# Kernel optimization log

Hardware: AMD Instinct MI355X
Metric: run time of the kernel (lower is better)

Reference implementation:

```python
import jax, jax.numpy as jnp
import numpy as np

NEG_SLOPE = 0.01  # torch nn.LeakyReLU default


def _lrelu(x):
    return jax.nn.leaky_relu(x, NEG_SLOPE)


def _conv1x1(x, w):
    # x: [B,C,H,W], w: [O,C] -> [B,O,H,W]  (1x1 conv, no bias)
    return jnp.einsum('bchw,oc->bohw', x, w)


def _distance_matrix(scale, H, W, dtype):
    # even-scale branch of the torch code
    x = jnp.arange(-(scale // 2), scale // 2 + 1, dtype=dtype)  # len scale+1
    x = jnp.concatenate([x[: (scale + 1) // 2], x[(scale + 1) // 2 + 1:]])  # drop middle -> len scale
    d0 = jnp.broadcast_to(x[None, :], (scale, scale))
    d1 = d0.T
    d2 = jnp.sqrt(d0 ** 2 + d1 ** 2)
    dm = jnp.stack([d0, d1, d2], axis=0)            # [3, s, s]
    dm = jnp.tile(dm, (1, H // scale, W // scale))   # [3, H, W]
    return dm[None]                                  # [1, 3, H, W]


def setup_inputs() -> dict:
    key = jax.random.key(0)
    ks = jax.random.split(key, 10)
    B, C, h, w, scale = 1, 16, 256, 256, 4
    H, W = h * scale, w * scale
    f32 = jnp.float32

    def kaiming(k, shape):
        fan_out = shape[0]
        std = np.sqrt(2.0 / fan_out)
        return (jax.random.normal(k, shape, dtype=f32) * std)

    return {
        'lr_feature': jax.random.normal(ks[0], (B, C, h, w), dtype=f32),
        'hr_feature': jax.random.normal(ks[1], (B, C, H, W), dtype=f32),
        'w0': kaiming(ks[2], (32, 64)),
        'w1': kaiming(ks[3], (16, 32)),
        'w2': kaiming(ks[4], (8, 16)),
        'w3': kaiming(ks[5], (1, 8)),
        's0': kaiming(ks[6], (3, 3)),
        's1': kaiming(ks[7], (2, 3)),
        's2': kaiming(ks[8], (1, 2)),
        'wf': jnp.abs(kaiming(ks[9], (1, 2))),
    }


def reference(lr_feature, hr_feature, w0, w1, w2, w3, s0, s1, s2, wf):
    B, C, h, w = lr_feature.shape
    H, W = hr_feature.shape[-2:]
    scale = W // w  # static under jit

    # nearest-neighbor expand of lr_feature to hr resolution
    lr_up = jnp.repeat(jnp.repeat(lr_feature, scale, axis=2), scale, axis=3)

    # representation: [B, 4C, H, W]
    rep = jnp.concatenate(
        [lr_up, hr_feature, lr_up * hr_feature, (lr_up - hr_feature) ** 2], axis=1)

    # similarity_measure1: 4C->32->16->8->1, leaky relu after each
    o = _lrelu(_conv1x1(rep, w0))
    o = _lrelu(_conv1x1(o, w1))
    o = _lrelu(_conv1x1(o, w2))
    weights1 = _lrelu(_conv1x1(o, w3))  # [B,1,H,W]

    # similarity_measure2 on the tiled distance matrix: 3->3->2->1
    dm = _distance_matrix(scale, H, W, lr_feature.dtype)  # [1,3,H,W]
    o2 = _lrelu(_conv1x1(dm, s0))
    o2 = _lrelu(_conv1x1(o2, s1))
    weights2 = _lrelu(_conv1x1(o2, s2))  # [1,1,H,W]

    # fuse with abs-constrained weights
    fused_in = jnp.concatenate([weights1, weights2], axis=1)  # [B,2,H,W] (B=1)
    mapping = _lrelu(_conv1x1(fused_in, jnp.abs(wf)))
    return mapping
```

## Files before the change

### kernel.cpp

```cpp
#include <hip/hip_runtime.h>
#include <hip/hip_bf16.h>


typedef __attribute__((ext_vector_type(8))) short bf16x8;
typedef __attribute__((ext_vector_type(4))) short s16x4;
typedef __attribute__((ext_vector_type(4))) float f32x4;

union B8 { bf16x8 v; short2 p[4]; };
union B4 { s16x4 v; short2 p[2]; };

__device__ __forceinline__ float lrelu(float x) { return fmaxf(x, 0.01f * x); }

__device__ __forceinline__ short2 cvt2(float a, float b) {
    __hip_bfloat162 h = __float22bfloat162_rn(make_float2(a, b));
    short2 s; __builtin_memcpy(&s, &h, 4); return s;
}

__global__ __launch_bounds__(256) void ctx_mfma(
    const float* __restrict__ lr,  const float* __restrict__ hr,
    const float* __restrict__ w0g, const float* __restrict__ w1g,
    const float* __restrict__ w2g, const float* __restrict__ w3g,
    const float* __restrict__ s0g, const float* __restrict__ s1g,
    const float* __restrict__ s2g, const float* __restrict__ wfg,
    float* __restrict__ out)
{
    constexpr int W = 1024, HW = 1024 * 1024, LHW = 256 * 256;
    __shared__ __align__(16) short zbuf[4][512];

    const int tid  = threadIdx.x;
    const int lane = tid & 63;
    const int widx = tid >> 6;
    const int g    = lane >> 4;
    const int px   = lane & 15;

    const int wave_id = blockIdx.x * 4 + widx;
    const int y  = wave_id >> 3;
    const int xw = (wave_id & 7) << 7;

    B8 a1[2][2];
    #pragma unroll
    for (int m = 0; m < 2; ++m)
        #pragma unroll
        for (int q = 0; q < 2; ++q) {
            const float* wp = w0g + (m * 16 + px) * 64 + q * 32 + g * 8;
            #pragma unroll
            for (int j = 0; j < 4; ++j) a1[m][q].p[j] = cvt2(wp[2 * j], wp[2 * j + 1]);
        }
    B8 a2;
    {
        const float* wp = w1g + px * 32 + g * 8;
        #pragma unroll
        for (int j = 0; j < 4; ++j) a2.p[j] = cvt2(wp[2 * j], wp[2 * j + 1]);
    }
    B8 a3;
    {
        const bool val = (px < 8) && (g < 2);
        const float* wp = w2g + (px & 7) * 16 + (g & 1) * 8;
        const short2 z2s = make_short2(0, 0);
        #pragma unroll
        for (int j = 0; j < 4; ++j) a3.p[j] = val ? cvt2(wp[2 * j], wp[2 * j + 1]) : z2s;
    }
    const float4 w3v = *(const float4*)(w3g + (g & 1) * 4);

    const int xi = px & 3, yi = y & 3;
    const float d0 = (float)xi + ((xi < 2) ? -2.f : -1.f);
    const float d1 = (float)yi + ((yi < 2) ? -2.f : -1.f);
    const float d2 = sqrtf(d0 * d0 + d1 * d1);
    const float q0 = lrelu(s0g[0] * d0 + s0g[1] * d1 + s0g[2] * d2);
    const float q1 = lrelu(s0g[3] * d0 + s0g[4] * d1 + s0g[5] * d2);
    const float q2 = lrelu(s0g[6] * d0 + s0g[7] * d1 + s0g[8] * d2);
    const float u0 = lrelu(s1g[0] * q0 + s1g[1] * q1 + s1g[2] * q2);
    const float u1 = lrelu(s1g[3] * q0 + s1g[4] * q1 + s1g[5] * q2);
    const float wt2 = lrelu(s2g[0] * u0 + s2g[1] * u1);
    const float awf0 = fabsf(wfg[0]), awf1 = fabsf(wfg[1]);

    const int s4  = (px ^ (px >> 2)) & 3;
    short* zb = &zbuf[widx][0];
    const int row = px * 32;
    const int wza = row + ((((g >> 1)       ^ s4) & 3) << 3) + ((g & 1) << 2);
    const int wzb = row + (((((g >> 1) + 2) ^ s4) & 3) << 3) + ((g & 1) << 2);
    const int rb2 = row + (((g       ^ s4) & 3) << 3);
    const int rb3 = row + ((((g & 1) ^ s4) & 3) << 3);

    const int cb = (g & 1) << 3;
    int hr_idx[8], lr_idx[8];
    #pragma unroll
    for (int j = 0; j < 8; ++j) {
        hr_idx[j] = (cb + j) * HW  + y * W + xw + px;
        lr_idx[j] = (cb + j) * LHW + (y >> 2) * 256 + (xw >> 2) + (px >> 2);
    }
    const int oidx = y * W + xw + px;
    const bool lo = (g < 2);
    const f32x4 zf = {0.f, 0.f, 0.f, 0.f};

    #pragma unroll
    for (int tt = 0; tt < 8; ++tt) {
        float lrv[8], hrv[8];
        #pragma unroll
        for (int j = 0; j < 8; ++j) {
            hrv[j] = hr[hr_idx[j] + tt * 16];
            lrv[j] = lr[lr_idx[j] + tt * 4];
        }
        B8 b0, b1;
        #pragma unroll
        for (int j = 0; j < 4; ++j) {
            float ua = lo ? lrv[2 * j]     : hrv[2 * j];
            float ub = lo ? lrv[2 * j + 1] : hrv[2 * j + 1];
            b0.p[j] = cvt2(ua, ub);
            float da = lrv[2 * j]     - hrv[2 * j];
            float db = lrv[2 * j + 1] - hrv[2 * j + 1];
            float pa = lo ? lrv[2 * j]     * hrv[2 * j]     : da * da;
            float pb = lo ? lrv[2 * j + 1] * hrv[2 * j + 1] : db * db;
            b1.p[j] = cvt2(pa, pb);
        }
        f32x4 acc1a = __builtin_amdgcn_mfma_f32_16x16x32_bf16(a1[0][0].v, b0.v, zf, 0, 0, 0);
        acc1a = __builtin_amdgcn_mfma_f32_16x16x32_bf16(a1[0][1].v, b1.v, acc1a, 0, 0, 0);
        f32x4 acc1b = __builtin_amdgcn_mfma_f32_16x16x32_bf16(a1[1][0].v, b0.v, zf, 0, 0, 0);
        acc1b = __builtin_amdgcn_mfma_f32_16x16x32_bf16(a1[1][1].v, b1.v, acc1b, 0, 0, 0);
        B4 za, zbp;
        za.p[0]  = cvt2(lrelu(acc1a.x), lrelu(acc1a.y));
        za.p[1]  = cvt2(lrelu(acc1a.z), lrelu(acc1a.w));
        zbp.p[0] = cvt2(lrelu(acc1b.x), lrelu(acc1b.y));
        zbp.p[1] = cvt2(lrelu(acc1b.z), lrelu(acc1b.w));
        *(s16x4*)&zb[wza] = za.v;
        *(s16x4*)&zb[wzb] = zbp.v;
        bf16x8 bz1 = *(const bf16x8*)&zb[rb2];
        f32x4 acc2 = __builtin_amdgcn_mfma_f32_16x16x32_bf16(a2.v, bz1, zf, 0, 0, 0);
        B4 z2p;
        z2p.p[0] = cvt2(lrelu(acc2.x), lrelu(acc2.y));
        z2p.p[1] = cvt2(lrelu(acc2.z), lrelu(acc2.w));
        *(s16x4*)&zb[wza] = z2p.v;
        bf16x8 bz2 = *(const bf16x8*)&zb[rb3];
        f32x4 acc3 = __builtin_amdgcn_mfma_f32_16x16x32_bf16(a3.v, bz2, zf, 0, 0, 0);
        float part = w3v.x * lrelu(acc3.x) + w3v.y * lrelu(acc3.y)
                   + w3v.z * lrelu(acc3.z) + w3v.w * lrelu(acc3.w);
        float sum = part + __shfl_xor(part, 16, 64);
        float wt1 = lrelu(sum);
        float res = lrelu(awf0 * wt1 + awf1 * wt2);
        if (g == 0) out[oidx + tt * 16] = res;
    }
}

extern "C" void kernel_launch(void* const* d_in, const int* in_sizes, int n_in,
                              void* d_out, int out_size, void* d_ws, size_t ws_size,
                              hipStream_t stream) {
    const float* lr = (const float*)d_in[0];
    const float* hr = (const float*)d_in[1];
    const float* w0 = (const float*)d_in[2];
    const float* w1 = (const float*)d_in[3];
    const float* w2 = (const float*)d_in[4];
    const float* w3 = (const float*)d_in[5];
    const float* s0 = (const float*)d_in[6];
    const float* s1 = (const float*)d_in[7];
    const float* s2 = (const float*)d_in[8];
    const float* wf = (const float*)d_in[9];
    float* o = (float*)d_out;

    ctx_mfma<<<2048, 256, 0, stream>>>(lr, hr, w0, w1, w2, w3, s0, s1, s2, wf, o);
}
```

Measured before the change: 142.6 us.

## Software-pipeline tile loads and double-buffer LDS scratch per wave

Restructures the per-wave loop to prefetch the next tile's hr/lr values into registers while the current tile is computed, alternating between two register sets. It adds a second LDS scratch buffer and moves the layer-2 output into its own swizzled region, so consecutive tiles no longer share LDS slots. This is meant to hide global load latency behind the MFMA chain and drop write-after-read hazards between tiles. The cost is more registers and more LDS per block, which could lower occupancy, though the loop was already fully unrolled and the compiler may have been overlapping loads before.

```diff
diff --git a/kernel.cpp b/kernel.cpp
--- a/kernel.cpp
+++ b/kernel.cpp
@@ -25,7 +25,8 @@
     float* __restrict__ out)
 {
     constexpr int W = 1024, HW = 1024 * 1024, LHW = 256 * 256;
-    __shared__ __align__(16) short zbuf[4][512];
+    __shared__ __align__(16) short zbufA[4][768];
+    __shared__ __align__(16) short zbufB[4][768];
 
     const int tid  = threadIdx.x;
     const int lane = tid & 63;
@@ -75,12 +76,15 @@
     const float awf0 = fabsf(wfg[0]), awf1 = fabsf(wfg[1]);
 
     const int s4  = (px ^ (px >> 2)) & 3;
-    short* zb = &zbuf[widx][0];
     const int row = px * 32;
     const int wza = row + ((((g >> 1)       ^ s4) & 3) << 3) + ((g & 1) << 2);
     const int wzb = row + (((((g >> 1) + 2) ^ s4) & 3) << 3) + ((g & 1) << 2);
     const int rb2 = row + (((g       ^ s4) & 3) << 3);
-    const int rb3 = row + ((((g & 1) ^ s4) & 3) << 3);
+    const int wz2 = 512 + px * 16 + (((g >> 1) ^ (px & 1)) << 3) + ((g & 1) << 2);
+    const int rz3 = 512 + px * 16 + ((((g & 1) ^ (px & 1)) & 1) << 3);
+
+    short* zbA = &zbufA[widx][0];
+    short* zbB = &zbufB[widx][0];
 
     const int cb = (g & 1) << 3;
     int hr_idx[8], lr_idx[8];
@@ -93,52 +97,67 @@
     const bool lo = (g < 2);
     const f32x4 zf = {0.f, 0.f, 0.f, 0.f};
 
+#define LOADT(LV, HV, T)                                                      \
+    {                                                                         \
+        _Pragma("unroll")                                                     \
+        for (int j = 0; j < 8; ++j) {                                         \
+            HV[j] = hr[hr_idx[j] + (T) * 16];                                 \
+            LV[j] = lr[lr_idx[j] + (T) * 4];                                  \
+        }                                                                     \
+    }
+
+#define COMPUTE(LV, HV, ZP, T)                                                \
+    {                                                                         \
+        B8 b0, b1;                                                            \
+        _Pragma("unroll")                                                     \
+        for (int j = 0; j < 4; ++j) {                                         \
+            float ua = lo ? LV[2 * j]     : HV[2 * j];                        \
+            float ub = lo ? LV[2 * j + 1] : HV[2 * j + 1];                    \
+            b0.p[j] = cvt2(ua, ub);                                           \
+            float da = LV[2 * j]     - HV[2 * j];                             \
+            float db = LV[2 * j + 1] - HV[2 * j + 1];                         \
+            float pa = lo ? LV[2 * j]     * HV[2 * j]     : da * da;          \
+            float pb = lo ? LV[2 * j + 1] * HV[2 * j + 1] : db * db;          \
+            b1.p[j] = cvt2(pa, pb);                                           \
+        }                                                                     \
+        f32x4 acc1a = __builtin_amdgcn_mfma_f32_16x16x32_bf16(a1[0][0].v, b0.v, zf, 0, 0, 0); \
+        acc1a = __builtin_amdgcn_mfma_f32_16x16x32_bf16(a1[0][1].v, b1.v, acc1a, 0, 0, 0);    \
+        f32x4 acc1b = __builtin_amdgcn_mfma_f32_16x16x32_bf16(a1[1][0].v, b0.v, zf, 0, 0, 0); \
+        acc1b = __builtin_amdgcn_mfma_f32_16x16x32_bf16(a1[1][1].v, b1.v, acc1b, 0, 0, 0);    \
+        B4 za, zq;                                                            \
+        za.p[0] = cvt2(lrelu(acc1a.x), lrelu(acc1a.y));                       \
+        za.p[1] = cvt2(lrelu(acc1a.z), lrelu(acc1a.w));                       \
+        zq.p[0] = cvt2(lrelu(acc1b.x), lrelu(acc1b.y));                       \
+        zq.p[1] = cvt2(lrelu(acc1b.z), lrelu(acc1b.w));                       \
+        *(s16x4*)&ZP[wza] = za.v;                                             \
+        *(s16x4*)&ZP[wzb] = zq.v;                                             \
+        bf16x8 bz1 = *(const bf16x8*)&ZP[rb2];                                \
+        f32x4 acc2 = __builtin_amdgcn_mfma_f32_16x16x32_bf16(a2.v, bz1, zf, 0, 0, 0); \
+        B4 z2q;                                                               \
+        z2q.p[0] = cvt2(lrelu(acc2.x), lrelu(acc2.y));                        \
+        z2q.p[1] = cvt2(lrelu(acc2.z), lrelu(acc2.w));                        \
+        *(s16x4*)&ZP[wz2] = z2q.v;                                            \
+        bf16x8 bz2 = *(const bf16x8*)&ZP[rz3];                                \
+        f32x4 acc3 = __builtin_amdgcn_mfma_f32_16x16x32_bf16(a3.v, bz2, zf, 0, 0, 0); \
+        float part = w3v.x * lrelu(acc3.x) + w3v.y * lrelu(acc3.y)            \
+                   + w3v.z * lrelu(acc3.z) + w3v.w * lrelu(acc3.w);           \
+        float sum = part + __shfl_xor(part, 16, 64);                          \
+        float wt1 = lrelu(sum);                                               \
+        float res = lrelu(awf0 * wt1 + awf1 * wt2);                           \
+        if (g == 0) out[oidx + (T) * 16] = res;                               \
+    }
+
+    float la[8], ha[8], lb[8], hb[8];
+    LOADT(la, ha, 0);
     #pragma unroll
-    for (int tt = 0; tt < 8; ++tt) {
-        float lrv[8], hrv[8];
-        #pragma unroll
-        for (int j = 0; j < 8; ++j) {
-            hrv[j] = hr[hr_idx[j] + tt * 16];
-            lrv[j] = lr[lr_idx[j] + tt * 4];
-        }
-        B8 b0, b1;
-        #pragma unroll
-        for (int j = 0; j < 4; ++j) {
-            float ua = lo ? lrv[2 * j]     : hrv[2 * j];
-            float ub = lo ? lrv[2 * j + 1] : hrv[2 * j + 1];
-            b0.p[j] = cvt2(ua, ub);
-            float da = lrv[2 * j]     - hrv[2 * j];
-            float db = lrv[2 * j + 1] - hrv[2 * j + 1];
-            float pa = lo ? lrv[2 * j]     * hrv[2 * j]     : da * da;
-            float pb = lo ? lrv[2 * j + 1] * hrv[2 * j + 1] : db * db;
-            b1.p[j] = cvt2(pa, pb);
-        }
-        f32x4 acc1a = __builtin_amdgcn_mfma_f32_16x16x32_bf16(a1[0][0].v, b0.v, zf, 0, 0, 0);
-        acc1a = __builtin_amdgcn_mfma_f32_16x16x32_bf16(a1[0][1].v, b1.v, acc1a, 0, 0, 0);
-        f32x4 acc1b = __builtin_amdgcn_mfma_f32_16x16x32_bf16(a1[1][0].v, b0.v, zf, 0, 0, 0);
-        acc1b = __builtin_amdgcn_mfma_f32_16x16x32_bf16(a1[1][1].v, b1.v, acc1b, 0, 0, 0);
-        B4 za, zbp;
-        za.p[0]  = cvt2(lrelu(acc1a.x), lrelu(acc1a.y));
-        za.p[1]  = cvt2(lrelu(acc1a.z), lrelu(acc1a.w));
-        zbp.p[0] = cvt2(lrelu(acc1b.x), lrelu(acc1b.y));
-        zbp.p[1] = cvt2(lrelu(acc1b.z), lrelu(acc1b.w));
-        *(s16x4*)&zb[wza] = za.v;
-        *(s16x4*)&zb[wzb] = zbp.v;
-        bf16x8 bz1 = *(const bf16x8*)&zb[rb2];
-        f32x4 acc2 = __builtin_amdgcn_mfma_f32_16x16x32_bf16(a2.v, bz1, zf, 0, 0, 0);
-        B4 z2p;
-        z2p.p[0] = cvt2(lrelu(acc2.x), lrelu(acc2.y));
-        z2p.p[1] = cvt2(lrelu(acc2.z), lrelu(acc2.w));
-        *(s16x4*)&zb[wza] = z2p.v;
-        bf16x8 bz2 = *(const bf16x8*)&zb[rb3];
-        f32x4 acc3 = __builtin_amdgcn_mfma_f32_16x16x32_bf16(a3.v, bz2, zf, 0, 0, 0);
-        float part = w3v.x * lrelu(acc3.x) + w3v.y * lrelu(acc3.y)
-                   + w3v.z * lrelu(acc3.z) + w3v.w * lrelu(acc3.w);
-        float sum = part + __shfl_xor(part, 16, 64);
-        float wt1 = lrelu(sum);
-        float res = lrelu(awf0 * wt1 + awf1 * wt2);
-        if (g == 0) out[oidx + tt * 16] = res;
+    for (int tt = 0; tt < 8; tt += 2) {
+        LOADT(lb, hb, tt + 1);
+        COMPUTE(la, ha, zbA, tt);
+        if (tt + 2 < 8) LOADT(la, ha, tt + 2);
+        COMPUTE(lb, hb, zbB, tt + 1);
     }
+#undef LOADT
+#undef COMPUTE
 }
 
 extern "C" void kernel_launch(void* const* d_in, const int* in_sizes, int n_in,
```

Result: faster. 138.4 us (-2.9%).

## Use 32x32 MFMA chain with permlane swaps and async LDS double-buffered hr loads

Applied to the files above, without the earlier changes.

Moves the per-pixel MLP from 16x16x32 MFMAs to 32x32x16 MFMAs so each wave handles 32 pixels per step. Inter-layer activations are re-laid out in registers with v_permlane32_swap instead of an LDS scratch round-trip. The hr tile is loaded with global_load_lds into a two-slot LDS buffer under manual vmcnt waits, and the lr values are preloaded into registers once. This aims to overlap memory traffic with compute and cut LDS shuffles, at the cost of fragile hand-written waitcnt ordering and more register pressure.

```diff
diff --git a/kernel.cpp b/kernel.cpp
--- a/kernel.cpp
+++ b/kernel.cpp
@@ -3,11 +3,9 @@
 
 
 typedef __attribute__((ext_vector_type(8))) short bf16x8;
-typedef __attribute__((ext_vector_type(4))) short s16x4;
-typedef __attribute__((ext_vector_type(4))) float f32x4;
-
-union B8 { bf16x8 v; short2 p[4]; };
-union B4 { s16x4 v; short2 p[2]; };
+typedef __attribute__((ext_vector_type(16))) float f32x16;
+
+union B8 { bf16x8 v; short2 p[4]; int d[4]; };
 
 __device__ __forceinline__ float lrelu(float x) { return fmaxf(x, 0.01f * x); }
 
@@ -15,6 +13,20 @@
     __hip_bfloat162 h = __float22bfloat162_rn(make_float2(a, b));
     short2 s; __builtin_memcpy(&s, &h, 4); return s;
 }
+__device__ __forceinline__ int pk(float a, float b) {
+    short2 s = cvt2(lrelu(a), lrelu(b));
+    int r; __builtin_memcpy(&r, &s, 4); return r;
+}
+
+__device__ __forceinline__ void gl16(const float* g, float* l) {
+    __builtin_amdgcn_global_load_lds(
+        (const __attribute__((address_space(1))) void*)g,
+        (__attribute__((address_space(3))) void*)l, 16, 0, 0);
+}
+
+#define SWAP32(x, y) asm("v_permlane32_swap_b32 %0, %1" : "+v"(x), "+v"(y))
+
+#define MFMA32(A, B, C) __builtin_amdgcn_mfma_f32_32x32x16_bf16((A), (B), (C), 0, 0, 0)
 
 __global__ __launch_bounds__(256) void ctx_mfma(
     const float* __restrict__ lr,  const float* __restrict__ hr,
@@ -25,42 +37,51 @@
     float* __restrict__ out)
 {
     constexpr int W = 1024, HW = 1024 * 1024, LHW = 256 * 256;
-    __shared__ __align__(16) short zbuf[4][512];
+
+    __shared__ __align__(16) float shr[4][2][512];
 
     const int tid  = threadIdx.x;
     const int lane = tid & 63;
     const int widx = tid >> 6;
-    const int g    = lane >> 4;
-    const int px   = lane & 15;
+    const int h    = lane >> 5;
+    const int px   = lane & 31;
+    const int cb   = h << 3;
 
     const int wave_id = blockIdx.x * 4 + widx;
     const int y  = wave_id >> 3;
     const int xw = (wave_id & 7) << 7;
 
-    B8 a1[2][2];
+    B8 a1[4];
     #pragma unroll
-    for (int m = 0; m < 2; ++m)
-        #pragma unroll
-        for (int q = 0; q < 2; ++q) {
-            const float* wp = w0g + (m * 16 + px) * 64 + q * 32 + g * 8;
+    for (int q = 0; q < 4; ++q)
+        #pragma unroll
+        for (int j = 0; j < 4; ++j) {
+            const float* wp = w0g + px * 64 + q * 16 + cb + 2 * j;
+            a1[q].p[j] = cvt2(wp[0], wp[1]);
+        }
+    B8 a2[2];
+    {
+        const bool v2 = (px < 16);
+        const short2 z2s = make_short2(0, 0);
+        #pragma unroll
+        for (int q = 0; q < 2; ++q)
             #pragma unroll
-            for (int j = 0; j < 4; ++j) a1[m][q].p[j] = cvt2(wp[2 * j], wp[2 * j + 1]);
-        }
-    B8 a2;
-    {
-        const float* wp = w1g + px * 32 + g * 8;
-        #pragma unroll
-        for (int j = 0; j < 4; ++j) a2.p[j] = cvt2(wp[2 * j], wp[2 * j + 1]);
+            for (int j = 0; j < 4; ++j) {
+                const float* wp = w1g + (px & 15) * 32 + q * 16 + cb + 2 * j;
+                a2[q].p[j] = v2 ? cvt2(wp[0], wp[1]) : z2s;
+            }
     }
     B8 a3;
     {
-        const bool val = (px < 8) && (g < 2);
-        const float* wp = w2g + (px & 7) * 16 + (g & 1) * 8;
+        const bool v3 = (px < 8);
         const short2 z2s = make_short2(0, 0);
         #pragma unroll
-        for (int j = 0; j < 4; ++j) a3.p[j] = val ? cvt2(wp[2 * j], wp[2 * j + 1]) : z2s;
-    }
-    const float4 w3v = *(const float4*)(w3g + (g & 1) * 4);
+        for (int j = 0; j < 4; ++j) {
+            const float* wp = w2g + (px & 7) * 16 + cb + 2 * j;
+            a3.p[j] = v3 ? cvt2(wp[0], wp[1]) : z2s;
+        }
+    }
+    const float4 w3v = *(const float4*)(w3g + h * 4);
 
     const int xi = px & 3, yi = y & 3;
     const float d0 = (float)xi + ((xi < 2) ? -2.f : -1.f);
@@ -74,71 +95,91 @@
     const float wt2 = lrelu(s2g[0] * u0 + s2g[1] * u1);
     const float awf0 = fabsf(wfg[0]), awf1 = fabsf(wfg[1]);
 
-    const int s4  = (px ^ (px >> 2)) & 3;
-    short* zb = &zbuf[widx][0];
-    const int row = px * 32;
-    const int wza = row + ((((g >> 1)       ^ s4) & 3) << 3) + ((g & 1) << 2);
-    const int wzb = row + (((((g >> 1) + 2) ^ s4) & 3) << 3) + ((g & 1) << 2);
-    const int rb2 = row + (((g       ^ s4) & 3) << 3);
-    const int rb3 = row + ((((g & 1) ^ s4) & 3) << 3);
-
-    const int cb = (g & 1) << 3;
-    int hr_idx[8], lr_idx[8];
+    float lrq[8][4];
+    const float* lrb = lr + (y >> 2) * 256 + (xw >> 2) + (px >> 2);
     #pragma unroll
-    for (int j = 0; j < 8; ++j) {
-        hr_idx[j] = (cb + j) * HW  + y * W + xw + px;
-        lr_idx[j] = (cb + j) * LHW + (y >> 2) * 256 + (xw >> 2) + (px >> 2);
-    }
+    for (int j = 0; j < 8; ++j)
+        #pragma unroll
+        for (int t = 0; t < 4; ++t)
+            lrq[j][t] = lrb[(cb + j) * LHW + t * 8];
+
+    const float* hrs = hr + (lane >> 3) * HW + y * W + xw + (lane & 7) * 4;
+    float* lds0 = &shr[widx][0][0];
+    float* lds1 = &shr[widx][1][0];
+
     const int oidx = y * W + xw + px;
-    const bool lo = (g < 2);
-    const f32x4 zf = {0.f, 0.f, 0.f, 0.f};
-
-    #pragma unroll
-    for (int tt = 0; tt < 8; ++tt) {
-        float lrv[8], hrv[8];
-        #pragma unroll
-        for (int j = 0; j < 8; ++j) {
-            hrv[j] = hr[hr_idx[j] + tt * 16];
-            lrv[j] = lr[lr_idx[j] + tt * 4];
-        }
-        B8 b0, b1;
-        #pragma unroll
-        for (int j = 0; j < 4; ++j) {
-            float ua = lo ? lrv[2 * j]     : hrv[2 * j];
-            float ub = lo ? lrv[2 * j + 1] : hrv[2 * j + 1];
-            b0.p[j] = cvt2(ua, ub);
-            float da = lrv[2 * j]     - hrv[2 * j];
-            float db = lrv[2 * j + 1] - hrv[2 * j + 1];
-            float pa = lo ? lrv[2 * j]     * hrv[2 * j]     : da * da;
-            float pb = lo ? lrv[2 * j + 1] * hrv[2 * j + 1] : db * db;
-            b1.p[j] = cvt2(pa, pb);
-        }
-        f32x4 acc1a = __builtin_amdgcn_mfma_f32_16x16x32_bf16(a1[0][0].v, b0.v, zf, 0, 0, 0);
-        acc1a = __builtin_amdgcn_mfma_f32_16x16x32_bf16(a1[0][1].v, b1.v, acc1a, 0, 0, 0);
-        f32x4 acc1b = __builtin_amdgcn_mfma_f32_16x16x32_bf16(a1[1][0].v, b0.v, zf, 0, 0, 0);
-        acc1b = __builtin_amdgcn_mfma_f32_16x16x32_bf16(a1[1][1].v, b1.v, acc1b, 0, 0, 0);
-        B4 za, zbp;
-        za.p[0]  = cvt2(lrelu(acc1a.x), lrelu(acc1a.y));
-        za.p[1]  = cvt2(lrelu(acc1a.z), lrelu(acc1a.w));
-        zbp.p[0] = cvt2(lrelu(acc1b.x), lrelu(acc1b.y));
-        zbp.p[1] = cvt2(lrelu(acc1b.z), lrelu(acc1b.w));
-        *(s16x4*)&zb[wza] = za.v;
-        *(s16x4*)&zb[wzb] = zbp.v;
-        bf16x8 bz1 = *(const bf16x8*)&zb[rb2];
-        f32x4 acc2 = __builtin_amdgcn_mfma_f32_16x16x32_bf16(a2.v, bz1, zf, 0, 0, 0);
-        B4 z2p;
-        z2p.p[0] = cvt2(lrelu(acc2.x), lrelu(acc2.y));
-        z2p.p[1] = cvt2(lrelu(acc2.z), lrelu(acc2.w));
-        *(s16x4*)&zb[wza] = z2p.v;
-        bf16x8 bz2 = *(const bf16x8*)&zb[rb3];
-        f32x4 acc3 = __builtin_amdgcn_mfma_f32_16x16x32_bf16(a3.v, bz2, zf, 0, 0, 0);
-        float part = w3v.x * lrelu(acc3.x) + w3v.y * lrelu(acc3.y)
-                   + w3v.z * lrelu(acc3.z) + w3v.w * lrelu(acc3.w);
-        float sum = part + __shfl_xor(part, 16, 64);
-        float wt1 = lrelu(sum);
-        float res = lrelu(awf0 * wt1 + awf1 * wt2);
-        if (g == 0) out[oidx + tt * 16] = res;
-    }
+    const f32x16 zf = {0.f};
+
+#define STAGE(LP, T)                                                          \
+    {                                                                         \
+        gl16(hrs + (T) * 32, (LP));                                           \
+        gl16(hrs + 8 * HW + (T) * 32, (LP) + 256);                            \
+    }
+
+#define COMP(LP, T)                                                          \
+    {                                                                         \
+        float hrv[8], lh[8], dd[8];                                          \
+        _Pragma("unroll")                                                    \
+        for (int j = 0; j < 8; ++j) hrv[j] = (LP)[(cb + j) * 32 + px];       \
+        _Pragma("unroll")                                                    \
+        for (int j = 0; j < 8; ++j) {                                        \
+            float lv = lrq[j][T];                                            \
+            lh[j] = lv * hrv[j];                                             \
+            float da = lv - hrv[j];                                          \
+            dd[j] = da * da;                                                 \
+        }                                                                    \
+        B8 b0, b1, b2, b3;                                                   \
+        _Pragma("unroll")                                                    \
+        for (int i = 0; i < 4; ++i) {                                        \
+            b0.p[i] = cvt2(lrq[2 * i][T], lrq[2 * i + 1][T]);                \
+            b1.p[i] = cvt2(hrv[2 * i], hrv[2 * i + 1]);                      \
+            b2.p[i] = cvt2(lh[2 * i], lh[2 * i + 1]);                        \
+            b3.p[i] = cvt2(dd[2 * i], dd[2 * i + 1]);                        \
+        }                                                                    \
+        f32x16 d1a = MFMA32(a1[0].v, b0.v, zf);                              \
+        d1a = MFMA32(a1[1].v, b1.v, d1a);                                    \
+        d1a = MFMA32(a1[2].v, b2.v, d1a);                                    \
+        d1a = MFMA32(a1[3].v, b3.v, d1a);                                    \
+                        \
+        int P0 = pk(d1a[0],  d1a[1]),  P1 = pk(d1a[2],  d1a[3]);             \
+        int P2 = pk(d1a[4],  d1a[5]),  P3 = pk(d1a[6],  d1a[7]);             \
+        int P4 = pk(d1a[8],  d1a[9]),  P5 = pk(d1a[10], d1a[11]);            \
+        int P6 = pk(d1a[12], d1a[13]), P7 = pk(d1a[14], d1a[15]);            \
+        SWAP32(P0, P2); SWAP32(P1, P3);          \
+        SWAP32(P4, P6); SWAP32(P5, P7);          \
+        B8 b2a, b2b;                                                         \
+        b2a.d[0] = P0; b2a.d[1] = P1; b2a.d[2] = P2; b2a.d[3] = P3;          \
+        b2b.d[0] = P4; b2b.d[1] = P5; b2b.d[2] = P6; b2b.d[3] = P7;          \
+        f32x16 d2a = MFMA32(a2[0].v, b2a.v, zf);                             \
+        d2a = MFMA32(a2[1].v, b2b.v, d2a);                                   \
+        int Q0 = pk(d2a[0], d2a[1]), Q1 = pk(d2a[2], d2a[3]);                \
+        int Q2 = pk(d2a[4], d2a[5]), Q3 = pk(d2a[6], d2a[7]);                \
+        SWAP32(Q0, Q2); SWAP32(Q1, Q3);                                      \
+        B8 b3f;                                                              \
+        b3f.d[0] = Q0; b3f.d[1] = Q1; b3f.d[2] = Q2; b3f.d[3] = Q3;          \
+        f32x16 d3a = MFMA32(a3.v, b3f.v, zf);                                \
+        float part = w3v.x * lrelu(d3a[0]) + w3v.y * lrelu(d3a[1])           \
+                   + w3v.z * lrelu(d3a[2]) + w3v.w * lrelu(d3a[3]);          \
+        float sum = part + __shfl_xor(part, 32, 64);                         \
+        float wt1 = lrelu(sum);                                              \
+        float res = lrelu(awf0 * wt1 + awf1 * wt2);                          \
+        if (lane < 32) out[oidx + (T) * 32] = res;                           \
+    }
+
+#define WAITV(N) asm volatile("s_waitcnt vmcnt(" #N ")" ::: "memory")
+
+    STAGE(lds0, 0)
+    STAGE(lds1, 1)
+    WAITV(2); COMP(lds0, 0)
+    STAGE(lds0, 2)
+    WAITV(3); COMP(lds1, 1)
+    STAGE(lds1, 3)
+    WAITV(3); COMP(lds0, 2)
+    WAITV(1); COMP(lds1, 3)
+
+#undef STAGE
+#undef COMP
+#undef WAITV
 }
 
 extern "C" void kernel_launch(void* const* d_in, const int* in_sizes, int n_in,
```

Result: faster. 135.9 us (-4.6%).
